# Performance work log

Measured on AMD Instinct MI355X. Metric: run time of the kernel, lower is better.

## Reference

```python
import jax, jax.numpy as jnp
import numpy as np

MAX_POINTS = 2048  # config['object_points']


def setup_inputs() -> dict:
    key = jax.random.key(0)
    k1, k2 = jax.random.split(key)
    B, N, C = 64, 131072, 4
    point_cloud = jax.random.normal(k1, (B, N, C), dtype=jnp.float32)
    logits = jax.random.normal(k2, (B, 2, N), dtype=jnp.float32)
    return {"point_cloud": point_cloud, "logits": logits}


def reference(point_cloud, logits):
    """JAX translation of point_cloud_masking.

    point_cloud: (B, N, C) with xyz in channels 0:3
    logits:      (B, 2, N)
    Returns (object_point_cloud (B, M, 3), mask_xyz_mean (B, 3)).
    """
    M = MAX_POINTS
    B, N, _ = point_cloud.shape
    dtype = point_cloud.dtype

    mask = logits[:, 0, :] < logits[:, 1, :]                  # (B, N) bool
    maskf = mask.astype(dtype)
    count_f = jnp.sum(maskf, axis=1)                          # (B,)
    xyz = point_cloud[..., :3]                                # (B, N, 3)
    mask_xyz_mean = jnp.sum(maskf[..., None] * xyz, axis=1) / jnp.maximum(count_f, 1.0)[:, None]  # (B,3)
    centered = xyz - mask_xyz_mean[:, None, :]                # (B, N, 3)

    # Stable argsort puts masked-point indices first, preserving order (like torch.where).
    order = jnp.argsort(1 - maskf, axis=1, stable=True)       # (B, N) int
    cnt = count_f.astype(jnp.int32)                           # (B,)

    # Resample to fixed M points (with replacement), matching torch.randint semantics:
    #   cnt >  M: all M indices random in [0, cnt)
    #   cnt <  M: first cnt identity, remaining random in [0, cnt)
    #   cnt == M: identity
    ksel = jax.random.key(42)
    rand = jax.random.randint(ksel, (B, M), 0, jnp.maximum(cnt, 1)[:, None])
    j = jnp.arange(M, dtype=jnp.int32)[None, :]               # (1, M)
    keep = (j < cnt[:, None]) & (cnt[:, None] <= M)
    sel = jnp.where(keep, j, rand)                            # (B, M) positions into sorted order
    idx = jnp.take_along_axis(order, sel, axis=1)             # (B, M) original point indices
    obj = jnp.take_along_axis(centered, idx[..., None], axis=1)  # (B, M, 3)

    # Empty-mask fallback: ones * batch_index (matches torch branch).
    empty = (cnt == 0)[:, None, None]
    batch_ids = jnp.arange(B, dtype=dtype)[:, None, None]
    obj = jnp.where(empty, jnp.ones_like(obj) * batch_ids, obj)
    return obj, mask_xyz_mean
```

## Files before the change

### kernel.cpp

```cpp
#include <hip/hip_runtime.h>
#include <stdint.h>

#define BATCH 64
#define NPTS  131072
#define MPTS  2048
#define WORDS_PB (NPTS / 64)
#define P1_BLOCKS 1024
#define P1_SPAN   8192
#define P1_ITERS  (P1_SPAN / 256)

struct U2 { uint32_t a, b; };

__host__ __device__ constexpr U2 tf2x32(uint32_t k0, uint32_t k1, uint32_t x0, uint32_t x1) {
  uint32_t ks0 = k0, ks1 = k1, ks2 = k0 ^ k1 ^ 0x1BD11BDAu;
  x0 += ks0; x1 += ks1;
  const int rotA[4] = {13, 15, 26, 6};
  const int rotB[4] = {17, 29, 16, 24};
  for (int r = 0; r < 4; ++r) { x0 += x1; x1 = (x1 << rotA[r]) | (x1 >> (32 - rotA[r])); x1 ^= x0; }
  x0 += ks1; x1 += ks2 + 1u;
  for (int r = 0; r < 4; ++r) { x0 += x1; x1 = (x1 << rotB[r]) | (x1 >> (32 - rotB[r])); x1 ^= x0; }
  x0 += ks2; x1 += ks0 + 2u;
  for (int r = 0; r < 4; ++r) { x0 += x1; x1 = (x1 << rotA[r]) | (x1 >> (32 - rotA[r])); x1 ^= x0; }
  x0 += ks0; x1 += ks1 + 3u;
  for (int r = 0; r < 4; ++r) { x0 += x1; x1 = (x1 << rotB[r]) | (x1 >> (32 - rotB[r])); x1 ^= x0; }
  x0 += ks1; x1 += ks2 + 4u;
  for (int r = 0; r < 4; ++r) { x0 += x1; x1 = (x1 << rotA[r]) | (x1 >> (32 - rotA[r])); x1 ^= x0; }
  x0 += ks2; x1 += ks0 + 5u;
  return U2{x0, x1};
}

__global__ __launch_bounds__(256) void pass1_kernel(
    const float4* __restrict__ pc, const float* __restrict__ lg,
    float* __restrict__ sums, unsigned long long* __restrict__ maskWords) {
  int g = blockIdx.x;
  int t = threadIdx.x;
  int lane = t & 63, wv = t >> 6;
  int b = g >> 4;
  size_t base = (size_t)g * P1_SPAN;
  size_t inb  = base & (NPTS - 1);
  const float*  l0g = lg + (size_t)b * (2 * NPTS) + inb;
  const float*  l1g = l0g + NPTS;
  const float4* pcg = pc + base;

  float sx = 0.f, sy = 0.f, sz = 0.f;
#pragma unroll 4
  for (int k = 0; k < P1_ITERS; ++k) {
    int idx = k * 256 + t;
    float a0 = l0g[idx];
    float a1 = l1g[idx];
    float4 q = pcg[idx];
    bool m = a0 < a1;
    unsigned long long bal = __ballot(m);
    if (lane == 0) maskWords[(base + idx) >> 6] = bal;
    if (m) { sx += q.x; sy += q.y; sz += q.z; }
  }

  for (int o = 32; o; o >>= 1) {
    sx += __shfl_down(sx, o, 64);
    sy += __shfl_down(sy, o, 64);
    sz += __shfl_down(sz, o, 64);
  }
  __shared__ float ssx[4], ssy[4], ssz[4];
  if (lane == 0) { ssx[wv] = sx; ssy[wv] = sy; ssz[wv] = sz; }
  __syncthreads();
  if (t == 0) {
    atomicAdd(&sums[b * 3 + 0], ssx[0] + ssx[1] + ssx[2] + ssx[3]);
    atomicAdd(&sums[b * 3 + 1], ssy[0] + ssy[1] + ssy[2] + ssy[3]);
    atomicAdd(&sums[b * 3 + 2], ssz[0] + ssz[1] + ssz[2] + ssz[3]);
  }
}

__global__ __launch_bounds__(256) void pass2_kernel(
    const unsigned long long* __restrict__ maskWords, const float* __restrict__ sums,
    uint32_t* __restrict__ wordOff, int* __restrict__ cnt,
    float* __restrict__ mean, float* __restrict__ out) {
  int b = blockIdx.x, t = threadIdx.x;
  int lane = t & 63, wv = t >> 6;
  const unsigned long long* mw = maskWords + (size_t)b * WORDS_PB;
  int base = t * 8;
  int p[8];
  int local = 0;
#pragma unroll
  for (int k = 0; k < 8; ++k) { p[k] = __popcll(mw[base + k]); local += p[k]; }

  int x = local;
#pragma unroll
  for (int o = 1; o < 64; o <<= 1) {
    int y = __shfl_up(x, o, 64);
    if (lane >= o) x += y;
  }
  __shared__ int wsum[4];
  if (lane == 63) wsum[wv] = x;
  __syncthreads();
  int add = 0;
#pragma unroll
  for (int u = 0; u < 4; ++u) add += (u < wv) ? wsum[u] : 0;
  int run = add + x - local;
  uint32_t* wo = wordOff + (size_t)b * WORDS_PB;
#pragma unroll
  for (int k = 0; k < 8; ++k) { wo[base + k] = (uint32_t)run; run += p[k]; }

  if (t == 0) {
    int ct = wsum[0] + wsum[1] + wsum[2] + wsum[3];
    cnt[b] = ct;
    float d  = fmaxf((float)ct, 1.0f);
    float mx = sums[b * 3 + 0] / d;
    float my = sums[b * 3 + 1] / d;
    float mz = sums[b * 3 + 2] / d;
    mean[b * 3 + 0] = mx; mean[b * 3 + 1] = my; mean[b * 3 + 2] = mz;
    float* om = out + (size_t)BATCH * MPTS * 3 + (size_t)b * 3;
    om[0] = mx; om[1] = my; om[2] = mz;
  }
}

__global__ __launch_bounds__(256) void pass3_kernel(
    const float4* __restrict__ pc, const int* __restrict__ cnt,
    const float* __restrict__ mean, const uint32_t* __restrict__ wordOff,
    const unsigned long long* __restrict__ maskWords,
    float* __restrict__ out) {
  int blk = blockIdx.x;
  int b = blk >> 3;
  int t = threadIdx.x;
  int j = (blk & 7) * 256 + t;
  int gid = b * MPTS + j;

  __shared__ uint32_t sOff[WORDS_PB];
  __shared__ float sMean[3];
  __shared__ int sCnt;
  const uint32_t* wo = wordOff + (size_t)b * WORDS_PB;
#pragma unroll
  for (int k = 0; k < 8; ++k) sOff[t + k * 256] = wo[t + k * 256];
  if (t < 3)  sMean[t] = mean[b * 3 + t];
  if (t == 0) sCnt = cnt[b];
  __syncthreads();

  int cb = sCnt;
  float ox, oy, oz;
  if (cb == 0) {
    ox = oy = oz = (float)b;
  } else {
    constexpr U2 K1 = tf2x32(0u, 42u, 0u, 0u);
    constexpr U2 K2 = tf2x32(0u, 42u, 0u, 1u);
    uint32_t span = (uint32_t)cb;
    U2 h = tf2x32(K1.a, K1.b, 0u, (uint32_t)gid);
    U2 l = tf2x32(K2.a, K2.b, 0u, (uint32_t)gid);
    uint32_t hb = h.a ^ h.b;
    uint32_t lb = l.a ^ l.b;
    uint32_t mul = 65536u % span;
    mul = (mul * mul) % span;
    uint32_t off = ((hb % span) * mul + (lb % span)) % span;
    int r = (j < cb && cb <= MPTS) ? j : (int)off;

    int lo = 0;
#pragma unroll
    for (int step = 1024; step; step >>= 1) {
      int nxt = lo + step;
      if (nxt < WORDS_PB && sOff[nxt] <= (uint32_t)r) lo = nxt;
    }
    int rem = r - (int)sOff[lo];
    unsigned long long w = maskWords[(size_t)b * WORDS_PB + lo];

    uint32_t cur = (uint32_t)w;
    int bitbase = 0;
    int c = __popc(cur);
    if (rem >= c) { rem -= c; cur = (uint32_t)(w >> 32); bitbase = 32; }
    c = __popc(cur & 0xFFFFu); if (rem >= c) { rem -= c; cur >>= 16; bitbase += 16; }
    c = __popc(cur & 0xFFu);   if (rem >= c) { rem -= c; cur >>= 8;  bitbase += 8;  }
    c = __popc(cur & 0xFu);    if (rem >= c) { rem -= c; cur >>= 4;  bitbase += 4;  }
    c = __popc(cur & 0x3u);    if (rem >= c) { rem -= c; cur >>= 2;  bitbase += 2;  }
    c = (int)(cur & 1u);       if (rem >= c) {           cur >>= 1;  bitbase += 1;  }
    int idx = lo * 64 + bitbase;

    float4 p = pc[(size_t)b * NPTS + idx];
    ox = p.x - sMean[0]; oy = p.y - sMean[1]; oz = p.z - sMean[2];
  }
  float* o = out + (size_t)gid * 3;
  o[0] = ox; o[1] = oy; o[2] = oz;
}

extern "C" void kernel_launch(void* const* d_in, const int* in_sizes, int n_in,
                              void* d_out, int out_size, void* d_ws, size_t ws_size,
                              hipStream_t stream) {
  const float4* pc = (const float4*)d_in[0];
  const float*  lg = (const float*)d_in[1];
  float* out = (float*)d_out;

  char* w = (char*)d_ws;
  float*    sums    = (float*)(w + 0);
  int*      cnt     = (int*)(w + 1024);
  float*    mean    = (float*)(w + 2048);
  uint32_t* wordOff = (uint32_t*)(w + 4096);
  unsigned long long* maskWords =
      (unsigned long long*)(w + 4096 + 524288);

  hipMemsetAsync(sums, 0, 768, stream);

  pass1_kernel<<<P1_BLOCKS, 256, 0, stream>>>(pc, lg, sums, maskWords);
  pass2_kernel<<<BATCH, 256, 0, stream>>>(maskWords, sums, wordOff, cnt, mean, out);
  pass3_kernel<<<(BATCH * MPTS) / 256, 256, 0, stream>>>(pc, cnt, mean, wordOff, maskWords, out);
}
```

Measured before the change: 246.4 us.

## Fuse three passes into one cooperative kernel with grid syncs and vectorized loads

Merges the mask/sum pass, the per-batch prefix-scan pass and the gather pass into a single cooperative kernel separated by grid.sync, which removes two kernel launches and the memset. Logits are now read as float4 with four ballots, and the bits are interleaved into the mask words through a spread operation. Atomic sum accumulation is replaced by per-block partial sums that are reduced later. In exchange, the kernel needs all 1024 blocks to be co-resident, pays for grid-wide barriers, and the scan phase runs on only 64 blocks while the others wait.

```diff
diff --git a/kernel.cpp b/kernel.cpp
--- a/kernel.cpp
+++ b/kernel.cpp
@@ -1,13 +1,16 @@
 #include <hip/hip_runtime.h>
+#include <hip/hip_cooperative_groups.h>
 #include <stdint.h>
+
+namespace cg = cooperative_groups;
 
 #define BATCH 64
 #define NPTS  131072
 #define MPTS  2048
 #define WORDS_PB (NPTS / 64)
-#define P1_BLOCKS 1024
-#define P1_SPAN   8192
-#define P1_ITERS  (P1_SPAN / 256)
+#define GRID_BLOCKS 1024
+#define SPAN  8192
+#define P1_ITERS (SPAN / 1024)
 
 struct U2 { uint32_t a, b; };
 
@@ -29,153 +32,187 @@
   return U2{x0, x1};
 }
 
-__global__ __launch_bounds__(256) void pass1_kernel(
+__device__ __forceinline__ unsigned long long spread4(unsigned long long x) {
+  x &= 0xFFFFull;
+  x = (x | (x << 24)) & 0x000000FF000000FFull;
+  x = (x | (x << 12)) & 0x000F000F000F000Full;
+  x = (x | (x << 6))  & 0x0303030303030303ull;
+  x = (x | (x << 3))  & 0x1111111111111111ull;
+  return x;
+}
+
+__global__ __launch_bounds__(256, 4) void fused_kernel(
     const float4* __restrict__ pc, const float* __restrict__ lg,
-    float* __restrict__ sums, unsigned long long* __restrict__ maskWords) {
-  int g = blockIdx.x;
-  int t = threadIdx.x;
-  int lane = t & 63, wv = t >> 6;
-  int b = g >> 4;
-  size_t base = (size_t)g * P1_SPAN;
-  size_t inb  = base & (NPTS - 1);
-  const float*  l0g = lg + (size_t)b * (2 * NPTS) + inb;
-  const float*  l1g = l0g + NPTS;
-  const float4* pcg = pc + base;
-
-  float sx = 0.f, sy = 0.f, sz = 0.f;
-#pragma unroll 4
-  for (int k = 0; k < P1_ITERS; ++k) {
-    int idx = k * 256 + t;
-    float a0 = l0g[idx];
-    float a1 = l1g[idx];
-    float4 q = pcg[idx];
-    bool m = a0 < a1;
-    unsigned long long bal = __ballot(m);
-    if (lane == 0) maskWords[(base + idx) >> 6] = bal;
-    if (m) { sx += q.x; sy += q.y; sz += q.z; }
+    float* __restrict__ out, float* __restrict__ sumsPartial,
+    int* __restrict__ cnt, float* __restrict__ mean,
+    uint32_t* __restrict__ wordOff, unsigned long long* __restrict__ maskWords) {
+  cg::grid_group grid = cg::this_grid();
+  const int g = blockIdx.x;
+  const int t = threadIdx.x;
+  const int lane = t & 63, wv = t >> 6;
+
+  __shared__ uint32_t sOff[WORDS_PB];
+
+  {
+    const int b = g >> 4;
+    const size_t base = (size_t)g * SPAN;
+    const size_t inb = base & (NPTS - 1);
+    const float4* l0v = (const float4*)(lg + (size_t)b * (2 * NPTS) + inb);
+    const float4* l1v = (const float4*)(lg + (size_t)b * (2 * NPTS) + NPTS + inb);
+    const float4* pcg = pc + base;
+
+    float sx = 0.f, sy = 0.f, sz = 0.f;
+#pragma unroll 2
+    for (int k = 0; k < P1_ITERS; ++k) {
+      const int i = k * 256 + t;
+      float4 a0 = l0v[i];
+      float4 a1 = l1v[i];
+      float4 p0 = pcg[4 * i + 0];
+      float4 p1 = pcg[4 * i + 1];
+      float4 p2 = pcg[4 * i + 2];
+      float4 p3 = pcg[4 * i + 3];
+      bool m0 = a0.x < a1.x, m1 = a0.y < a1.y, m2 = a0.z < a1.z, m3 = a0.w < a1.w;
+      unsigned long long B0 = __ballot(m0);
+      unsigned long long B1 = __ballot(m1);
+      unsigned long long B2 = __ballot(m2);
+      unsigned long long B3 = __ballot(m3);
+      if ((lane & 15) == 0) {
+        const int w = lane >> 4;
+        const int sh = 16 * w;
+        unsigned long long word = spread4((B0 >> sh) & 0xFFFFull)
+                                | (spread4((B1 >> sh) & 0xFFFFull) << 1)
+                                | (spread4((B2 >> sh) & 0xFFFFull) << 2)
+                                | (spread4((B3 >> sh) & 0xFFFFull) << 3);
+        maskWords[(base + (size_t)k * 1024 + (size_t)wv * 256 + (size_t)w * 64) >> 6] = word;
+      }
+      if (m0) { sx += p0.x; sy += p0.y; sz += p0.z; }
+      if (m1) { sx += p1.x; sy += p1.y; sz += p1.z; }
+      if (m2) { sx += p2.x; sy += p2.y; sz += p2.z; }
+      if (m3) { sx += p3.x; sy += p3.y; sz += p3.z; }
+    }
+
+    for (int o = 32; o; o >>= 1) {
+      sx += __shfl_down(sx, o, 64);
+      sy += __shfl_down(sy, o, 64);
+      sz += __shfl_down(sz, o, 64);
+    }
+    __shared__ float ssx[4], ssy[4], ssz[4];
+    if (lane == 0) { ssx[wv] = sx; ssy[wv] = sy; ssz[wv] = sz; }
+    __syncthreads();
+    if (t == 0) {
+      sumsPartial[g * 3 + 0] = ssx[0] + ssx[1] + ssx[2] + ssx[3];
+      sumsPartial[g * 3 + 1] = ssy[0] + ssy[1] + ssy[2] + ssy[3];
+      sumsPartial[g * 3 + 2] = ssz[0] + ssz[1] + ssz[2] + ssz[3];
+    }
   }
 
-  for (int o = 32; o; o >>= 1) {
-    sx += __shfl_down(sx, o, 64);
-    sy += __shfl_down(sy, o, 64);
-    sz += __shfl_down(sz, o, 64);
+  __threadfence();
+  grid.sync();
+
+  if (g < BATCH) {
+    const int b = g;
+    const unsigned long long* mw = maskWords + (size_t)b * WORDS_PB;
+    const int basew = t * 8;
+    int p[8];
+    int local = 0;
+#pragma unroll
+    for (int k = 0; k < 8; ++k) { p[k] = __popcll(mw[basew + k]); local += p[k]; }
+
+    int x = local;
+#pragma unroll
+    for (int o = 1; o < 64; o <<= 1) {
+      int y = __shfl_up(x, o, 64);
+      if (lane >= o) x += y;
+    }
+    __shared__ int wsum[4];
+    if (lane == 63) wsum[wv] = x;
+    __syncthreads();
+    int add = 0;
+#pragma unroll
+    for (int u = 0; u < 4; ++u) add += (u < wv) ? wsum[u] : 0;
+    int run = add + x - local;
+    uint32_t* wo = wordOff + (size_t)b * WORDS_PB;
+#pragma unroll
+    for (int k = 0; k < 8; ++k) { wo[basew + k] = (uint32_t)run; run += p[k]; }
+
+    if (t == 0) {
+      const int ct = wsum[0] + wsum[1] + wsum[2] + wsum[3];
+      cnt[b] = ct;
+      float sx = 0.f, sy = 0.f, sz = 0.f;
+#pragma unroll
+      for (int i = 0; i < 16; ++i) {
+        sx += sumsPartial[(b * 16 + i) * 3 + 0];
+        sy += sumsPartial[(b * 16 + i) * 3 + 1];
+        sz += sumsPartial[(b * 16 + i) * 3 + 2];
+      }
+      const float d = fmaxf((float)ct, 1.0f);
+      const float mx = sx / d, my = sy / d, mz = sz / d;
+      mean[b * 3 + 0] = mx; mean[b * 3 + 1] = my; mean[b * 3 + 2] = mz;
+      float* om = out + (size_t)BATCH * MPTS * 3 + (size_t)b * 3;
+      om[0] = mx; om[1] = my; om[2] = mz;
+    }
   }
-  __shared__ float ssx[4], ssy[4], ssz[4];
-  if (lane == 0) { ssx[wv] = sx; ssy[wv] = sy; ssz[wv] = sz; }
-  __syncthreads();
-  if (t == 0) {
-    atomicAdd(&sums[b * 3 + 0], ssx[0] + ssx[1] + ssx[2] + ssx[3]);
-    atomicAdd(&sums[b * 3 + 1], ssy[0] + ssy[1] + ssy[2] + ssy[3]);
-    atomicAdd(&sums[b * 3 + 2], ssz[0] + ssz[1] + ssz[2] + ssz[3]);
+
+  __threadfence();
+  grid.sync();
+
+  if (g < (BATCH * MPTS) / 256) {
+    const int b = g >> 3;
+    const int j = (g & 7) * 256 + t;
+    const int gid = b * MPTS + j;
+
+    const uint32_t* wo = wordOff + (size_t)b * WORDS_PB;
+#pragma unroll
+    for (int k = 0; k < 8; ++k) sOff[t + k * 256] = wo[t + k * 256];
+    __shared__ float sMean[3];
+    __shared__ int sCnt;
+    if (t < 3)  sMean[t] = mean[b * 3 + t];
+    if (t == 0) sCnt = cnt[b];
+    __syncthreads();
+
+    const int cb = sCnt;
+    float ox, oy, oz;
+    if (cb == 0) {
+      ox = oy = oz = (float)b;
+    } else {
+      constexpr U2 K1 = tf2x32(0u, 42u, 0u, 0u);
+      constexpr U2 K2 = tf2x32(0u, 42u, 0u, 1u);
+      const uint32_t span = (uint32_t)cb;
+      U2 h = tf2x32(K1.a, K1.b, 0u, (uint32_t)gid);
+      U2 l = tf2x32(K2.a, K2.b, 0u, (uint32_t)gid);
+      uint32_t hb = h.a ^ h.b;
+      uint32_t lb = l.a ^ l.b;
+      uint32_t mul = 65536u % span;
+      mul = (mul * mul) % span;
+      uint32_t off = ((hb % span) * mul + (lb % span)) % span;
+      int r = (j < cb && cb <= MPTS) ? j : (int)off;
+
+      int lo = 0;
+#pragma unroll
+      for (int step = 1024; step; step >>= 1) {
+        int nxt = lo + step;
+        if (nxt < WORDS_PB && sOff[nxt] <= (uint32_t)r) lo = nxt;
+      }
+      int rem = r - (int)sOff[lo];
+      unsigned long long w = maskWords[(size_t)b * WORDS_PB + lo];
+
+      uint32_t cur = (uint32_t)w;
+      int bitbase = 0;
+      int c = __popc(cur);
+      if (rem >= c) { rem -= c; cur = (uint32_t)(w >> 32); bitbase = 32; }
+      c = __popc(cur & 0xFFFFu); if (rem >= c) { rem -= c; cur >>= 16; bitbase += 16; }
+      c = __popc(cur & 0xFFu);   if (rem >= c) { rem -= c; cur >>= 8;  bitbase += 8;  }
+      c = __popc(cur & 0xFu);    if (rem >= c) { rem -= c; cur >>= 4;  bitbase += 4;  }
+      c = __popc(cur & 0x3u);    if (rem >= c) { rem -= c; cur >>= 2;  bitbase += 2;  }
+      c = (int)(cur & 1u);       if (rem >= c) {           cur >>= 1;  bitbase += 1;  }
+      const int idx = lo * 64 + bitbase;
+
+      float4 p = pc[(size_t)b * NPTS + idx];
+      ox = p.x - sMean[0]; oy = p.y - sMean[1]; oz = p.z - sMean[2];
+    }
+    float* o = out + (size_t)gid * 3;
+    o[0] = ox; o[1] = oy; o[2] = oz;
   }
-}
-
-__global__ __launch_bounds__(256) void pass2_kernel(
-    const unsigned long long* __restrict__ maskWords, const float* __restrict__ sums,
-    uint32_t* __restrict__ wordOff, int* __restrict__ cnt,
-    float* __restrict__ mean, float* __restrict__ out) {
-  int b = blockIdx.x, t = threadIdx.x;
-  int lane = t & 63, wv = t >> 6;
-  const unsigned long long* mw = maskWords + (size_t)b * WORDS_PB;
-  int base = t * 8;
-  int p[8];
-  int local = 0;
-#pragma unroll
-  for (int k = 0; k < 8; ++k) { p[k] = __popcll(mw[base + k]); local += p[k]; }
-
-  int x = local;
-#pragma unroll
-  for (int o = 1; o < 64; o <<= 1) {
-    int y = __shfl_up(x, o, 64);
-    if (lane >= o) x += y;
-  }
-  __shared__ int wsum[4];
-  if (lane == 63) wsum[wv] = x;
-  __syncthreads();
-  int add = 0;
-#pragma unroll
-  for (int u = 0; u < 4; ++u) add += (u < wv) ? wsum[u] : 0;
-  int run = add + x - local;
-  uint32_t* wo = wordOff + (size_t)b * WORDS_PB;
-#pragma unroll
-  for (int k = 0; k < 8; ++k) { wo[base + k] = (uint32_t)run; run += p[k]; }
-
-  if (t == 0) {
-    int ct = wsum[0] + wsum[1] + wsum[2] + wsum[3];
-    cnt[b] = ct;
-    float d  = fmaxf((float)ct, 1.0f);
-    float mx = sums[b * 3 + 0] / d;
-    float my = sums[b * 3 + 1] / d;
-    float mz = sums[b * 3 + 2] / d;
-    mean[b * 3 + 0] = mx; mean[b * 3 + 1] = my; mean[b * 3 + 2] = mz;
-    float* om = out + (size_t)BATCH * MPTS * 3 + (size_t)b * 3;
-    om[0] = mx; om[1] = my; om[2] = mz;
-  }
-}
-
-__global__ __launch_bounds__(256) void pass3_kernel(
-    const float4* __restrict__ pc, const int* __restrict__ cnt,
-    const float* __restrict__ mean, const uint32_t* __restrict__ wordOff,
-    const unsigned long long* __restrict__ maskWords,
-    float* __restrict__ out) {
-  int blk = blockIdx.x;
-  int b = blk >> 3;
-  int t = threadIdx.x;
-  int j = (blk & 7) * 256 + t;
-  int gid = b * MPTS + j;
-
-  __shared__ uint32_t sOff[WORDS_PB];
-  __shared__ float sMean[3];
-  __shared__ int sCnt;
-  const uint32_t* wo = wordOff + (size_t)b * WORDS_PB;
-#pragma unroll
-  for (int k = 0; k < 8; ++k) sOff[t + k * 256] = wo[t + k * 256];
-  if (t < 3)  sMean[t] = mean[b * 3 + t];
-  if (t == 0) sCnt = cnt[b];
-  __syncthreads();
-
-  int cb = sCnt;
-  float ox, oy, oz;
-  if (cb == 0) {
-    ox = oy = oz = (float)b;
-  } else {
-    constexpr U2 K1 = tf2x32(0u, 42u, 0u, 0u);
-    constexpr U2 K2 = tf2x32(0u, 42u, 0u, 1u);
-    uint32_t span = (uint32_t)cb;
-    U2 h = tf2x32(K1.a, K1.b, 0u, (uint32_t)gid);
-    U2 l = tf2x32(K2.a, K2.b, 0u, (uint32_t)gid);
-    uint32_t hb = h.a ^ h.b;
-    uint32_t lb = l.a ^ l.b;
-    uint32_t mul = 65536u % span;
-    mul = (mul * mul) % span;
-    uint32_t off = ((hb % span) * mul + (lb % span)) % span;
-    int r = (j < cb && cb <= MPTS) ? j : (int)off;
-
-    int lo = 0;
-#pragma unroll
-    for (int step = 1024; step; step >>= 1) {
-      int nxt = lo + step;
-      if (nxt < WORDS_PB && sOff[nxt] <= (uint32_t)r) lo = nxt;
-    }
-    int rem = r - (int)sOff[lo];
-    unsigned long long w = maskWords[(size_t)b * WORDS_PB + lo];
-
-    uint32_t cur = (uint32_t)w;
-    int bitbase = 0;
-    int c = __popc(cur);
-    if (rem >= c) { rem -= c; cur = (uint32_t)(w >> 32); bitbase = 32; }
-    c = __popc(cur & 0xFFFFu); if (rem >= c) { rem -= c; cur >>= 16; bitbase += 16; }
-    c = __popc(cur & 0xFFu);   if (rem >= c) { rem -= c; cur >>= 8;  bitbase += 8;  }
-    c = __popc(cur & 0xFu);    if (rem >= c) { rem -= c; cur >>= 4;  bitbase += 4;  }
-    c = __popc(cur & 0x3u);    if (rem >= c) { rem -= c; cur >>= 2;  bitbase += 2;  }
-    c = (int)(cur & 1u);       if (rem >= c) {           cur >>= 1;  bitbase += 1;  }
-    int idx = lo * 64 + bitbase;
-
-    float4 p = pc[(size_t)b * NPTS + idx];
-    ox = p.x - sMean[0]; oy = p.y - sMean[1]; oz = p.z - sMean[2];
-  }
-  float* o = out + (size_t)gid * 3;
-  o[0] = ox; o[1] = oy; o[2] = oz;
 }
 
 extern "C" void kernel_launch(void* const* d_in, const int* in_sizes, int n_in,
@@ -186,16 +223,17 @@
   float* out = (float*)d_out;
 
   char* w = (char*)d_ws;
-  float*    sums    = (float*)(w + 0);
-  int*      cnt     = (int*)(w + 1024);
-  float*    mean    = (float*)(w + 2048);
-  uint32_t* wordOff = (uint32_t*)(w + 4096);
+  float*    sumsPartial = (float*)(w + 0);
+  int*      cnt         = (int*)(w + 12288);
+  float*    mean        = (float*)(w + 12544);
+  uint32_t* wordOff     = (uint32_t*)(w + 13312);
   unsigned long long* maskWords =
-      (unsigned long long*)(w + 4096 + 524288);
-
-  hipMemsetAsync(sums, 0, 768, stream);
-
-  pass1_kernel<<<P1_BLOCKS, 256, 0, stream>>>(pc, lg, sums, maskWords);
-  pass2_kernel<<<BATCH, 256, 0, stream>>>(maskWords, sums, wordOff, cnt, mean, out);
-  pass3_kernel<<<(BATCH * MPTS) / 256, 256, 0, stream>>>(pc, cnt, mean, wordOff, maskWords, out);
-}
+      (unsigned long long*)(w + 537600);
+
+  void* args[] = {
+    (void*)&pc, (void*)&lg, (void*)&out, (void*)&sumsPartial,
+    (void*)&cnt, (void*)&mean, (void*)&wordOff, (void*)&maskWords
+  };
+  hipLaunchCooperativeKernel((void*)fused_kernel, dim3(GRID_BLOCKS), dim3(256),
+                             args, 0, stream);
+}
```

After: 658.6 us. 2.67x slower.

## Fuse prefix-scan pass into gather kernel, drop memset and atomics

Applied to the files above, without the earlier changes.

The separate per-batch prefix-scan kernel is removed. Every gather block now loads its batch's mask words into shared memory, recomputes the word offsets and count, and reduces per-block partial xyz sums to get the mean. Pass 1 writes its partial sums to dedicated slots instead of using atomics, which removes the memset, and it doubles the block count and batches four loads per iteration to keep more memory requests in flight. The cost is that the scan work is repeated eight times per batch and shared-memory use per gather block goes up.

```diff
diff --git a/kernel.cpp b/kernel.cpp
--- a/kernel.cpp
+++ b/kernel.cpp
@@ -5,9 +5,9 @@
 #define NPTS  131072
 #define MPTS  2048
 #define WORDS_PB (NPTS / 64)
-#define P1_BLOCKS 1024
-#define P1_SPAN   8192
-#define P1_ITERS  (P1_SPAN / 256)
+#define P1_BLOCKS 2048
+#define SPAN  4096
+#define P1_ITERS (SPAN / 1024)
 
 struct U2 { uint32_t a, b; };
 
@@ -29,30 +29,39 @@
   return U2{x0, x1};
 }
 
-__global__ __launch_bounds__(256) void pass1_kernel(
+__global__ __launch_bounds__(256, 4) void pass1_kernel(
     const float4* __restrict__ pc, const float* __restrict__ lg,
-    float* __restrict__ sums, unsigned long long* __restrict__ maskWords) {
-  int g = blockIdx.x;
-  int t = threadIdx.x;
-  int lane = t & 63, wv = t >> 6;
-  int b = g >> 4;
-  size_t base = (size_t)g * P1_SPAN;
-  size_t inb  = base & (NPTS - 1);
+    float* __restrict__ sumsPartial, unsigned long long* __restrict__ maskWords) {
+  const int g = blockIdx.x;
+  const int t = threadIdx.x;
+  const int lane = t & 63, wv = t >> 6;
+  const int b = g >> 5;
+  const size_t base = (size_t)g * SPAN;
+  const size_t inb  = base & (NPTS - 1);
   const float*  l0g = lg + (size_t)b * (2 * NPTS) + inb;
   const float*  l1g = l0g + NPTS;
   const float4* pcg = pc + base;
 
   float sx = 0.f, sy = 0.f, sz = 0.f;
-#pragma unroll 4
+#pragma unroll 2
   for (int k = 0; k < P1_ITERS; ++k) {
-    int idx = k * 256 + t;
-    float a0 = l0g[idx];
-    float a1 = l1g[idx];
-    float4 q = pcg[idx];
-    bool m = a0 < a1;
-    unsigned long long bal = __ballot(m);
-    if (lane == 0) maskWords[(base + idx) >> 6] = bal;
-    if (m) { sx += q.x; sy += q.y; sz += q.z; }
+    float a0q[4], a1q[4];
+    float4 pq[4];
+#pragma unroll
+    for (int q = 0; q < 4; ++q) {
+      const int idx = k * 1024 + q * 256 + t;
+      a0q[q] = l0g[idx];
+      a1q[q] = l1g[idx];
+      pq[q]  = pcg[idx];
+    }
+#pragma unroll
+    for (int q = 0; q < 4; ++q) {
+      const bool m = a0q[q] < a1q[q];
+      const unsigned long long bal = __ballot(m);
+      if (lane == 0)
+        maskWords[(base + (size_t)(k * 1024 + q * 256 + wv * 64)) >> 6] = bal;
+      if (m) { sx += pq[q].x; sy += pq[q].y; sz += pq[q].z; }
+    }
   }
 
   for (int o = 32; o; o >>= 1) {
@@ -64,84 +73,87 @@
   if (lane == 0) { ssx[wv] = sx; ssy[wv] = sy; ssz[wv] = sz; }
   __syncthreads();
   if (t == 0) {
-    atomicAdd(&sums[b * 3 + 0], ssx[0] + ssx[1] + ssx[2] + ssx[3]);
-    atomicAdd(&sums[b * 3 + 1], ssy[0] + ssy[1] + ssy[2] + ssy[3]);
-    atomicAdd(&sums[b * 3 + 2], ssz[0] + ssz[1] + ssz[2] + ssz[3]);
-  }
-}
-
-__global__ __launch_bounds__(256) void pass2_kernel(
-    const unsigned long long* __restrict__ maskWords, const float* __restrict__ sums,
-    uint32_t* __restrict__ wordOff, int* __restrict__ cnt,
-    float* __restrict__ mean, float* __restrict__ out) {
-  int b = blockIdx.x, t = threadIdx.x;
-  int lane = t & 63, wv = t >> 6;
+    sumsPartial[g * 3 + 0] = ssx[0] + ssx[1] + ssx[2] + ssx[3];
+    sumsPartial[g * 3 + 1] = ssy[0] + ssy[1] + ssy[2] + ssy[3];
+    sumsPartial[g * 3 + 2] = ssz[0] + ssz[1] + ssz[2] + ssz[3];
+  }
+}
+
+__global__ __launch_bounds__(256) void pass3_kernel(
+    const float4* __restrict__ pc, const float* __restrict__ sumsPartial,
+    const unsigned long long* __restrict__ maskWords,
+    float* __restrict__ out) {
+  const int blk = blockIdx.x;
+  const int b = blk >> 3;
+  const int t = threadIdx.x;
+  const int lane = t & 63, wv = t >> 6;
+  const int j = (blk & 7) * 256 + t;
+  const int gid = b * MPTS + j;
+
+  __shared__ unsigned long long sW[WORDS_PB];
+  __shared__ uint32_t sOff[WORDS_PB];
+  __shared__ int wsum[4];
+  __shared__ float sMean[3];
+  __shared__ int sCnt;
+
   const unsigned long long* mw = maskWords + (size_t)b * WORDS_PB;
-  int base = t * 8;
+#pragma unroll
+  for (int k = 0; k < 8; ++k) sW[t + k * 256] = mw[t + k * 256];
+  __syncthreads();
+
+  const int basew = t * 8;
   int p[8];
   int local = 0;
 #pragma unroll
-  for (int k = 0; k < 8; ++k) { p[k] = __popcll(mw[base + k]); local += p[k]; }
+  for (int k = 0; k < 8; ++k) { p[k] = __popcll(sW[basew + k]); local += p[k]; }
 
   int x = local;
 #pragma unroll
   for (int o = 1; o < 64; o <<= 1) {
-    int y = __shfl_up(x, o, 64);
+    const int y = __shfl_up(x, o, 64);
     if (lane >= o) x += y;
   }
-  __shared__ int wsum[4];
   if (lane == 63) wsum[wv] = x;
   __syncthreads();
   int add = 0;
 #pragma unroll
   for (int u = 0; u < 4; ++u) add += (u < wv) ? wsum[u] : 0;
   int run = add + x - local;
-  uint32_t* wo = wordOff + (size_t)b * WORDS_PB;
-#pragma unroll
-  for (int k = 0; k < 8; ++k) { wo[base + k] = (uint32_t)run; run += p[k]; }
-
-  if (t == 0) {
-    int ct = wsum[0] + wsum[1] + wsum[2] + wsum[3];
-    cnt[b] = ct;
-    float d  = fmaxf((float)ct, 1.0f);
-    float mx = sums[b * 3 + 0] / d;
-    float my = sums[b * 3 + 1] / d;
-    float mz = sums[b * 3 + 2] / d;
-    mean[b * 3 + 0] = mx; mean[b * 3 + 1] = my; mean[b * 3 + 2] = mz;
-    float* om = out + (size_t)BATCH * MPTS * 3 + (size_t)b * 3;
-    om[0] = mx; om[1] = my; om[2] = mz;
-  }
-}
-
-__global__ __launch_bounds__(256) void pass3_kernel(
-    const float4* __restrict__ pc, const int* __restrict__ cnt,
-    const float* __restrict__ mean, const uint32_t* __restrict__ wordOff,
-    const unsigned long long* __restrict__ maskWords,
-    float* __restrict__ out) {
-  int blk = blockIdx.x;
-  int b = blk >> 3;
-  int t = threadIdx.x;
-  int j = (blk & 7) * 256 + t;
-  int gid = b * MPTS + j;
-
-  __shared__ uint32_t sOff[WORDS_PB];
-  __shared__ float sMean[3];
-  __shared__ int sCnt;
-  const uint32_t* wo = wordOff + (size_t)b * WORDS_PB;
-#pragma unroll
-  for (int k = 0; k < 8; ++k) sOff[t + k * 256] = wo[t + k * 256];
-  if (t < 3)  sMean[t] = mean[b * 3 + t];
-  if (t == 0) sCnt = cnt[b];
-  __syncthreads();
-
-  int cb = sCnt;
+#pragma unroll
+  for (int k = 0; k < 8; ++k) { sOff[basew + k] = (uint32_t)run; run += p[k]; }
+
+  if (t < 64) {
+    float px = 0.f, py = 0.f, pz = 0.f;
+    if (t < 32) {
+      const float* sp = sumsPartial + ((size_t)b * 32 + t) * 3;
+      px = sp[0]; py = sp[1]; pz = sp[2];
+    }
+    for (int o = 32; o; o >>= 1) {
+      px += __shfl_down(px, o, 64);
+      py += __shfl_down(py, o, 64);
+      pz += __shfl_down(pz, o, 64);
+    }
+    if (t == 0) {
+      const int ct = wsum[0] + wsum[1] + wsum[2] + wsum[3];
+      sCnt = ct;
+      const float d = fmaxf((float)ct, 1.0f);
+      sMean[0] = px / d; sMean[1] = py / d; sMean[2] = pz / d;
+      if ((blk & 7) == 0) {
+        float* om = out + (size_t)BATCH * MPTS * 3 + (size_t)b * 3;
+        om[0] = sMean[0]; om[1] = sMean[1]; om[2] = sMean[2];
+      }
+    }
+  }
+  __syncthreads();
+
+  const int cb = sCnt;
   float ox, oy, oz;
   if (cb == 0) {
     ox = oy = oz = (float)b;
   } else {
     constexpr U2 K1 = tf2x32(0u, 42u, 0u, 0u);
     constexpr U2 K2 = tf2x32(0u, 42u, 0u, 1u);
-    uint32_t span = (uint32_t)cb;
+    const uint32_t span = (uint32_t)cb;
     U2 h = tf2x32(K1.a, K1.b, 0u, (uint32_t)gid);
     U2 l = tf2x32(K2.a, K2.b, 0u, (uint32_t)gid);
     uint32_t hb = h.a ^ h.b;
@@ -154,11 +166,11 @@
     int lo = 0;
 #pragma unroll
     for (int step = 1024; step; step >>= 1) {
-      int nxt = lo + step;
+      const int nxt = lo + step;
       if (nxt < WORDS_PB && sOff[nxt] <= (uint32_t)r) lo = nxt;
     }
     int rem = r - (int)sOff[lo];
-    unsigned long long w = maskWords[(size_t)b * WORDS_PB + lo];
+    const unsigned long long w = sW[lo];
 
     uint32_t cur = (uint32_t)w;
     int bitbase = 0;
@@ -169,10 +181,10 @@
     c = __popc(cur & 0xFu);    if (rem >= c) { rem -= c; cur >>= 4;  bitbase += 4;  }
     c = __popc(cur & 0x3u);    if (rem >= c) { rem -= c; cur >>= 2;  bitbase += 2;  }
     c = (int)(cur & 1u);       if (rem >= c) {           cur >>= 1;  bitbase += 1;  }
-    int idx = lo * 64 + bitbase;
-
-    float4 p = pc[(size_t)b * NPTS + idx];
-    ox = p.x - sMean[0]; oy = p.y - sMean[1]; oz = p.z - sMean[2];
+    const int idx = lo * 64 + bitbase;
+
+    const float4 pnt = pc[(size_t)b * NPTS + idx];
+    ox = pnt.x - sMean[0]; oy = pnt.y - sMean[1]; oz = pnt.z - sMean[2];
   }
   float* o = out + (size_t)gid * 3;
   o[0] = ox; o[1] = oy; o[2] = oz;
@@ -186,16 +198,10 @@
   float* out = (float*)d_out;
 
   char* w = (char*)d_ws;
-  float*    sums    = (float*)(w + 0);
-  int*      cnt     = (int*)(w + 1024);
-  float*    mean    = (float*)(w + 2048);
-  uint32_t* wordOff = (uint32_t*)(w + 4096);
+  float* sumsPartial = (float*)(w + 0);
   unsigned long long* maskWords =
-      (unsigned long long*)(w + 4096 + 524288);
-
-  hipMemsetAsync(sums, 0, 768, stream);
-
-  pass1_kernel<<<P1_BLOCKS, 256, 0, stream>>>(pc, lg, sums, maskWords);
-  pass2_kernel<<<BATCH, 256, 0, stream>>>(maskWords, sums, wordOff, cnt, mean, out);
-  pass3_kernel<<<(BATCH * MPTS) / 256, 256, 0, stream>>>(pc, cnt, mean, wordOff, maskWords, out);
-}
+      (unsigned long long*)(w + 24576);
+
+  pass1_kernel<<<P1_BLOCKS, 256, 0, stream>>>(pc, lg, sumsPartial, maskWords);
+  pass3_kernel<<<(BATCH * MPTS) / 256, 256, 0, stream>>>(pc, sumsPartial, maskWords, out);
+}
```

Result: faster. 239.4 us (-2.9%).
